# Optimization experiments

Measured on AMD Instinct MI355X. Metric: run time of the kernel, lower is better.

The kernel has to match this reference:

```python
import jax, jax.numpy as jnp
import numpy as np

N = 100000   # nodes
E = 1600000  # edges
IN = 64      # in_channels
H = 128      # hidden_features
G = 1024     # graphs in batch
NUM_REST = 3 # num_layers (extra GraphConv layers)


def setup_inputs() -> dict:
    key = jax.random.key(0)
    ks = jax.random.split(key, 12)
    x = jax.random.normal(ks[0], (N, IN), jnp.float32)
    edge_index = jax.random.randint(ks[1], (2, E), 0, N)
    edge_attr = jax.random.uniform(ks[2], (E,), jnp.float32)
    batch = jnp.sort(jax.random.randint(ks[3], (N,), 0, G))

    def glorot(k, shape, fan_in):
        return jax.random.normal(k, shape, jnp.float32) / np.float32(np.sqrt(fan_in))

    # GraphConv layer 0: in -> hidden (lin_root: no bias, lin_rel: bias)
    W_root0 = glorot(ks[4], (H, IN), IN)
    W_rel0 = glorot(ks[5], (H, IN), IN)
    b0 = jnp.zeros((H,), jnp.float32)
    # GraphConv layers 1..3: hidden -> hidden (stacked)
    W_root_r = glorot(ks[6], (NUM_REST, H, H), H)
    W_rel_r = glorot(ks[7], (NUM_REST, H, H), H)
    b_r = jnp.zeros((NUM_REST, H), jnp.float32)
    # MLPReadout: [H -> H//2 -> 1]
    Wr1 = glorot(ks[8], (H // 2, H), H)
    br1 = jnp.zeros((H // 2,), jnp.float32)
    Wr2 = glorot(ks[9], (1, H // 2), H // 2)
    br2 = jnp.zeros((1,), jnp.float32)
    return dict(x=x, edge_index=edge_index, edge_attr=edge_attr, batch=batch,
                W_root0=W_root0, W_rel0=W_rel0, b0=b0,
                W_root_r=W_root_r, W_rel_r=W_rel_r, b_r=b_r,
                Wr1=Wr1, br1=br1, Wr2=Wr2, br2=br2)


def graph_conv(x, src, dst, ew, W_root, W_rel, b):
    # PyG GraphConv (aggr='add'):
    #   out_i = W_rel @ sum_{j->i} e_ji * x_j + b + W_root @ x_i
    msg = ew[:, None] * x[src]                                   # [E, d]
    agg = jax.ops.segment_sum(msg, dst, num_segments=x.shape[0])  # [N, d]
    return agg @ W_rel.T + b + x @ W_root.T


def reference(x, edge_index, edge_attr, batch,
              W_root0, W_rel0, b0, W_root_r, W_rel_r, b_r,
              Wr1, br1, Wr2, br2):
    src, dst = edge_index[0], edge_index[1]
    y = graph_conv(x, src, dst, edge_attr, W_root0, W_rel0, b0)
    for l in range(W_root_r.shape[0]):
        y = graph_conv(y, src, dst, edge_attr, W_root_r[l], W_rel_r[l], b_r[l])
    # MLPReadout: Linear -> ReLU -> Linear
    y = jax.nn.relu(y @ Wr1.T + br1)
    y = y @ Wr2.T + br2                                           # [N, 1]
    # scatter-mean over graph assignment
    num = jax.ops.segment_sum(y, batch, num_segments=G)           # [G, 1]
    cnt = jax.ops.segment_sum(jnp.ones((y.shape[0], 1), y.dtype), batch,
                              num_segments=G)
    return num / jnp.maximum(cnt, 1.0)                            # [G, 1]
```

## Files before the change

### kernel.cpp

```cpp
#include <hip/hip_runtime.h>
#include <hip/hip_fp16.h>
#include <cstdint>
#include <cstddef>

#define NNODES 100000
#define NEDGES 1600000
#define NGRAPH 1024
#define NB_SCAN ((NNODES + 255) / 256)
#define FILL_CHUNK 4096
#define FILL_NCHUNK ((NEDGES + FILL_CHUNK - 1) / FILL_CHUNK)
#define SHARD 12500

typedef __attribute__((ext_vector_type(8))) short short8;
typedef __attribute__((ext_vector_type(8))) unsigned short ushort8;
typedef __attribute__((ext_vector_type(4))) float f32x4;

__device__ inline float b2f(unsigned short u) {
  return __uint_as_float(((unsigned int)u) << 16);
}
__device__ inline unsigned short f2b(float f) {
  unsigned int x = __float_as_uint(f);
  x += 0x7fffu + ((x >> 16) & 1u);
  return (unsigned short)(x >> 16);
}
__device__ inline unsigned int pack_edge(int src, float w) {
  unsigned short hb = __half_as_ushort(__float2half_rn(w));
  return ((unsigned int)src << 15) | ((unsigned int)hb >> 1);
}
__device__ inline void unpack_edge(unsigned int p, int& src, float& w) {
  src = (int)(p >> 15);
  w = __half2float(__ushort_as_half((unsigned short)((p & 0x7fffu) << 1)));
}

__global__ __launch_bounds__(256) void prepack_kernel(
    const float* __restrict__ Wrel0, const float* __restrict__ Wroot0,
    const float* __restrict__ WrelR, const float* __restrict__ WrootR,
    const float* __restrict__ Wr1, unsigned short* __restrict__ dst)
{
  int g = blockIdx.x * 256 + threadIdx.x;
  if (g >= 15360) return;
  const float* src; int H, K, r; unsigned short* out;
  if (g < 1024)       { src = Wrel0;  H = 128; K = 64;  r = g;        out = dst + r * 8; }
  else if (g < 2048)  { src = Wroot0; H = 128; K = 64;  r = g - 1024; out = dst + 8192 + r * 8; }
  else if (g < 8192)  { int m = g - 2048; int l = m / 2048; r = m % 2048;
                        src = WrelR + l * 16384;  H = 128; K = 128;
                        out = dst + 16384 + l * 16384 + r * 8; }
  else if (g < 14336) { int m = g - 8192; int l = m / 2048; r = m % 2048;
                        src = WrootR + l * 16384; H = 128; K = 128;
                        out = dst + 65536 + l * 16384 + r * 8; }
  else                { src = Wr1;    H = 64;  K = 128; r = g - 14336; out = dst + 114688 + r * 8; }
  int n = r % H, k8 = r / H;
  const float* s = src + (size_t)n * K + k8 * 8;
#pragma unroll
  for (int j = 0; j < 8; j++) out[j] = f2b(s[j]);
}

__global__ __launch_bounds__(256) void cvt_x_kernel(
    const float* __restrict__ x, unsigned short* __restrict__ xb)
{
  int i = blockIdx.x * 256 + threadIdx.x;
  if (i * 4 >= NNODES * 64) return;
  float4 v = *(const float4*)(x + i * 4);
  ushort4 o;
  o.x = f2b(v.x); o.y = f2b(v.y); o.z = f2b(v.z); o.w = f2b(v.w);
  *(ushort4*)(xb + i * 4) = o;
}

__global__ __launch_bounds__(256) void hist_kernel(
    const int* __restrict__ ei, int* __restrict__ deg)
{
  int e = blockIdx.x * 256 + threadIdx.x;
  if (e < NEDGES) atomicAdd(&deg[ei[NEDGES + e]], 1);
}

__global__ __launch_bounds__(256) void scan1_kernel(
    const int* __restrict__ deg, int* __restrict__ exloc, int* __restrict__ bsum)
{
  __shared__ int s[256];
  int i = blockIdx.x * 256 + threadIdx.x;
  int v = (i < NNODES) ? deg[i] : 0;
  s[threadIdx.x] = v;
  __syncthreads();
#pragma unroll
  for (int off = 1; off < 256; off <<= 1) {
    int t = (threadIdx.x >= off) ? s[threadIdx.x - off] : 0;
    __syncthreads();
    s[threadIdx.x] += t;
    __syncthreads();
  }
  if (i < NNODES) exloc[i] = s[threadIdx.x] - v;
  if (threadIdx.x == 255) bsum[blockIdx.x] = s[255];
}

__global__ __launch_bounds__(512) void scan2_kernel(int* __restrict__ bsum)
{
  __shared__ int s[512];
  int v = (threadIdx.x < NB_SCAN) ? bsum[threadIdx.x] : 0;
  s[threadIdx.x] = v;
  __syncthreads();
#pragma unroll
  for (int off = 1; off < 512; off <<= 1) {
    int t = (threadIdx.x >= off) ? s[threadIdx.x - off] : 0;
    __syncthreads();
    s[threadIdx.x] += t;
    __syncthreads();
  }
  if (threadIdx.x < NB_SCAN) bsum[threadIdx.x] = s[threadIdx.x] - v;
}

__global__ __launch_bounds__(256) void scan3_kernel(
    const int* __restrict__ exloc, const int* __restrict__ bsum,
    int* __restrict__ row_ptr, int* __restrict__ row_fill)
{
  int i = blockIdx.x * 256 + threadIdx.x;
  if (i < NNODES) {
    int v = exloc[i] + bsum[blockIdx.x];
    row_ptr[i] = v;
    row_fill[i] = v;
  }
  if (i == 0) row_ptr[NNODES] = NEDGES;
}

__global__ __launch_bounds__(256) void fill_kernel(
    const int* __restrict__ ei, const float* __restrict__ ew,
    int* __restrict__ row_fill, unsigned int* __restrict__ epack)
{
  int chunk = blockIdx.x >> 3;
  int shard = blockIdx.x & 7;
  int base = chunk * FILL_CHUNK;
  for (int t = threadIdx.x; t < FILL_CHUNK; t += 256) {
    int e = base + t;
    if (e >= NEDGES) break;
    int d = ei[NEDGES + e];
    if ((unsigned)d / SHARD == (unsigned)shard) {
      int p = atomicAdd(&row_fill[d], 1);
      epack[p] = pack_edge(ei[e], ew[e]);
    }
  }
}

__global__ __launch_bounds__(256) void gptr_kernel(
    const int* __restrict__ batch, int* __restrict__ gptr)
{
  int i = blockIdx.x * 256 + threadIdx.x;
  if (i >= NNODES) return;
  int b = batch[i];
  int bn = (i + 1 < NNODES) ? batch[i + 1] : NGRAPH;
  for (int g = b + 1; g <= bn; g++) gptr[g] = i + 1;
  if (i == 0) for (int g = 0; g <= b; g++) gptr[g] = 0;
}

__global__ __launch_bounds__(256) void agg128_kernel(
    const int* __restrict__ row_ptr, const unsigned int* __restrict__ epack,
    const unsigned short* __restrict__ x, unsigned short* __restrict__ agg)
{
  int node = blockIdx.x * 4 + (threadIdx.x >> 6);
  int lane = threadIdx.x & 63;
  if (node >= NNODES) return;
  int q = lane >> 4, sl = lane & 15;
  int s = row_ptr[node], e = row_ptr[node + 1];
  float acc[8];
#pragma unroll
  for (int j = 0; j < 8; j++) acc[j] = 0.f;

  for (int i = s + q; i < e; i += 16) {
    unsigned int p0 = epack[i];
    unsigned int p1 = (i + 4  < e) ? epack[i + 4]  : 0u;
    unsigned int p2 = (i + 8  < e) ? epack[i + 8]  : 0u;
    unsigned int p3 = (i + 12 < e) ? epack[i + 12] : 0u;
    int s0, s1, s2, s3; float w0, w1, w2, w3;
    unpack_edge(p0, s0, w0);
    unpack_edge(p1, s1, w1);
    unpack_edge(p2, s2, w2);
    unpack_edge(p3, s3, w3);
    ushort8 r0 = *(const ushort8*)(x + (size_t)s0 * 128 + sl * 8);
    ushort8 r1 = *(const ushort8*)(x + (size_t)s1 * 128 + sl * 8);
    ushort8 r2 = *(const ushort8*)(x + (size_t)s2 * 128 + sl * 8);
    ushort8 r3 = *(const ushort8*)(x + (size_t)s3 * 128 + sl * 8);
#pragma unroll
    for (int j = 0; j < 8; j++)
      acc[j] += w0 * b2f(r0[j]) + w1 * b2f(r1[j]) +
                w2 * b2f(r2[j]) + w3 * b2f(r3[j]);
  }
#pragma unroll
  for (int j = 0; j < 8; j++) {
    acc[j] += __shfl_xor(acc[j], 16, 64);
    acc[j] += __shfl_xor(acc[j], 32, 64);
  }
  if (q == 0) {
    ushort8 o;
#pragma unroll
    for (int j = 0; j < 8; j++) o[j] = f2b(acc[j]);
    *(ushort8*)(agg + (size_t)node * 128 + sl * 8) = o;
  }
}

__global__ __launch_bounds__(256) void agg64_kernel(
    const int* __restrict__ row_ptr, const unsigned int* __restrict__ epack,
    const unsigned short* __restrict__ x, unsigned short* __restrict__ agg)
{
  int node = blockIdx.x * 4 + (threadIdx.x >> 6);
  int lane = threadIdx.x & 63;
  if (node >= NNODES) return;
  int q = lane >> 3, sl = lane & 7;
  int s = row_ptr[node], e = row_ptr[node + 1];
  float acc[8];
#pragma unroll
  for (int j = 0; j < 8; j++) acc[j] = 0.f;

  for (int i = s + q; i < e; i += 16) {
    unsigned int p0 = epack[i];
    unsigned int p1 = (i + 8 < e) ? epack[i + 8] : 0u;
    int s0, s1; float w0, w1;
    unpack_edge(p0, s0, w0);
    unpack_edge(p1, s1, w1);
    ushort8 r0 = *(const ushort8*)(x + (size_t)s0 * 64 + sl * 8);
    ushort8 r1 = *(const ushort8*)(x + (size_t)s1 * 64 + sl * 8);
#pragma unroll
    for (int j = 0; j < 8; j++)
      acc[j] += w0 * b2f(r0[j]) + w1 * b2f(r1[j]);
  }
#pragma unroll
  for (int j = 0; j < 8; j++) {
    acc[j] += __shfl_xor(acc[j], 8, 64);
    acc[j] += __shfl_xor(acc[j], 16, 64);
    acc[j] += __shfl_xor(acc[j], 32, 64);
  }
  if (q == 0) {
    ushort8 o;
#pragma unroll
    for (int j = 0; j < 8; j++) o[j] = f2b(acc[j]);
    *(ushort8*)(agg + (size_t)node * 64 + sl * 8) = o;
  }
}

template <int KDIM, int HOUT, int MT, bool DUAL, bool RELU>
__global__ __launch_bounds__(256) void mfma_gemm(
    const unsigned short* __restrict__ A1, const unsigned short* __restrict__ W1,
    const unsigned short* __restrict__ A2, const unsigned short* __restrict__ W2,
    const float* __restrict__ bias, unsigned short* __restrict__ out)
{
  constexpr int NT2 = HOUT / 16;
  constexpr int KC = KDIM / 32;
  const int wave = threadIdx.x >> 6, lane = threadIdx.x & 63;
  const int quad = lane >> 4, l16 = lane & 15;
  const int n0 = (blockIdx.x * 4 + wave) * (MT * 16);

  f32x4 acc[MT][NT2];
#pragma unroll
  for (int m = 0; m < MT; m++)
#pragma unroll
    for (int t = 0; t < NT2; t++) acc[m][t] = (f32x4){0.f, 0.f, 0.f, 0.f};

  int nodes[MT];
#pragma unroll
  for (int m = 0; m < MT; m++) {
    int nd = n0 + m * 16 + l16;
    nodes[m] = nd < NNODES ? nd : NNODES - 1;
  }

#pragma unroll
  for (int c = 0; c < KC; c++) {
    short8 bfr[NT2];
#pragma unroll
    for (int t = 0; t < NT2; t++)
      bfr[t] = *(const short8*)(W1 + ((size_t)(c * 4 + quad) * HOUT + t * 16 + l16) * 8);
#pragma unroll
    for (int m = 0; m < MT; m++) {
      short8 af = *(const short8*)(A1 + (size_t)nodes[m] * KDIM + c * 32 + quad * 8);
#pragma unroll
      for (int t = 0; t < NT2; t++)
        acc[m][t] = __builtin_amdgcn_mfma_f32_16x16x32_bf16(af, bfr[t], acc[m][t], 0, 0, 0);
    }
    if (DUAL) {
#pragma unroll
      for (int t = 0; t < NT2; t++)
        bfr[t] = *(const short8*)(W2 + ((size_t)(c * 4 + quad) * HOUT + t * 16 + l16) * 8);
#pragma unroll
      for (int m = 0; m < MT; m++) {
        short8 af = *(const short8*)(A2 + (size_t)nodes[m] * KDIM + c * 32 + quad * 8);
#pragma unroll
        for (int t = 0; t < NT2; t++)
          acc[m][t] = __builtin_amdgcn_mfma_f32_16x16x32_bf16(af, bfr[t], acc[m][t], 0, 0, 0);
      }
    }
  }

#pragma unroll
  for (int m = 0; m < MT; m++) {
    int rowbase = n0 + m * 16 + quad * 4;
#pragma unroll
    for (int t = 0; t < NT2; t++) {
      float b = bias[t * 16 + l16];
#pragma unroll
      for (int r = 0; r < 4; r++) {
        int nd = rowbase + r;
        if (nd < NNODES) {
          float v = acc[m][t][r] + b;
          if (RELU) v = fmaxf(v, 0.f);
          out[(size_t)nd * HOUT + t * 16 + l16] = f2b(v);
        }
      }
    }
  }
}

__global__ __launch_bounds__(256) void readout_reduce_kernel(
    const unsigned short* __restrict__ h, const float* __restrict__ Wr2,
    const float* __restrict__ br2, const int* __restrict__ gptr,
    float* __restrict__ out)
{
  __shared__ float wsum[4];
  int g = blockIdx.x;
  int s = gptr[g], e = gptr[g + 1];
  int wave = threadIdx.x >> 6, lane = threadIdx.x & 63;
  float w2 = Wr2[lane];
  float acc = 0.f;
  for (int n = s + wave; n < e; n += 4)
    acc += b2f(h[(size_t)n * 64 + lane]) * w2;
#pragma unroll
  for (int off = 32; off >= 1; off >>= 1) acc += __shfl_xor(acc, off, 64);
  if (lane == 0) wsum[wave] = acc;
  __syncthreads();
  if (threadIdx.x == 0) {
    float cnt = (float)(e - s);
    float sum = wsum[0] + wsum[1] + wsum[2] + wsum[3] + cnt * br2[0];
    out[g] = sum / fmaxf(cnt, 1.f);
  }
}

extern "C" void kernel_launch(void* const* d_in, const int* in_sizes, int n_in,
                              void* d_out, int out_size, void* d_ws, size_t ws_size,
                              hipStream_t stream)
{
  const float* x      = (const float*)d_in[0];
  const int*   ei     = (const int*)d_in[1];
  const float* ew     = (const float*)d_in[2];
  const int*   batch  = (const int*)d_in[3];
  const float* Wroot0 = (const float*)d_in[4];
  const float* Wrel0  = (const float*)d_in[5];
  const float* b0     = (const float*)d_in[6];
  const float* WrootR = (const float*)d_in[7];
  const float* WrelR  = (const float*)d_in[8];
  const float* bR     = (const float*)d_in[9];
  const float* Wr1    = (const float*)d_in[10];
  const float* br1    = (const float*)d_in[11];
  const float* Wr2    = (const float*)d_in[12];
  const float* br2    = (const float*)d_in[13];

  char* ws = (char*)d_ws;
  unsigned short* wp   = (unsigned short*)ws;
  unsigned short* xb   = wp + 131072;
  unsigned short* agg0 = xb + (size_t)NNODES * 64;
  unsigned short* bufA = agg0 + (size_t)NNODES * 64;
  unsigned short* bufB = bufA + (size_t)NNODES * 128;
  unsigned short* hbuf = bufB + (size_t)NNODES * 128;
  int*  deg      = (int*)(hbuf + (size_t)NNODES * 64);
  int*  exloc    = deg + NNODES;
  int*  row_ptr  = exloc + NNODES;
  int*  row_fill = row_ptr + NNODES + 2;
  int*  bsum     = row_fill + NNODES;
  int*  gptr     = bsum + 512;
  unsigned int* epack = (unsigned int*)(gptr + NGRAPH + 2);

  prepack_kernel<<<60, 256, 0, stream>>>(Wrel0, Wroot0, WrelR, WrootR, Wr1, wp);
  cvt_x_kernel<<<(NNODES * 64 / 4 + 255) / 256, 256, 0, stream>>>(x, xb);

  const unsigned short* pWrel0  = wp;
  const unsigned short* pWroot0 = wp + 8192;
  const unsigned short* pWrelR  = wp + 16384;
  const unsigned short* pWrootR = wp + 65536;
  const unsigned short* pWr1    = wp + 114688;

  hipMemsetAsync(deg, 0, NNODES * sizeof(int), stream);
  hist_kernel<<<(NEDGES + 255) / 256, 256, 0, stream>>>(ei, deg);
  scan1_kernel<<<NB_SCAN, 256, 0, stream>>>(deg, exloc, bsum);
  scan2_kernel<<<1, 512, 0, stream>>>(bsum);
  scan3_kernel<<<NB_SCAN, 256, 0, stream>>>(exloc, bsum, row_ptr, row_fill);
  fill_kernel<<<FILL_NCHUNK * 8, 256, 0, stream>>>(ei, ew, row_fill, epack);
  gptr_kernel<<<(NNODES + 255) / 256, 256, 0, stream>>>(batch, gptr);

  agg64_kernel<<<(NNODES + 3) / 4, 256, 0, stream>>>(row_ptr, epack, xb, agg0);
  mfma_gemm<64, 128, 2, true, false><<<(NNODES + 127) / 128, 256, 0, stream>>>(
      agg0, pWrel0, xb, pWroot0, b0, bufB);

  unsigned short* bufs[2] = { bufB, bufA };
  for (int l = 0; l < 3; l++) {
    unsigned short* in  = bufs[l & 1];
    unsigned short* agg = bufs[(l & 1) ^ 1];
    agg128_kernel<<<(NNODES + 3) / 4, 256, 0, stream>>>(row_ptr, epack, in, agg);
    mfma_gemm<128, 128, 2, true, false><<<(NNODES + 127) / 128, 256, 0, stream>>>(
        agg, pWrelR + l * 16384, in, pWrootR + l * 16384, bR + l * 128, agg);
  }

  mfma_gemm<128, 64, 4, false, true><<<(NNODES + 255) / 256, 256, 0, stream>>>(
      bufA, pWr1, nullptr, nullptr, br1, hbuf);
  readout_reduce_kernel<<<NGRAPH, 256, 0, stream>>>(hbuf, Wr2, br2, gptr, (float*)d_out);
}
```

Measured before the change: 596.4 us.

## Replace atomic CSR build with two-level bucket counting sort

Swaps the global-atomic histogram, three-pass scan and sharded atomic fill for a two-level counting sort. Edges are first binned into 256-node buckets using per-chunk shared-memory histograms, then scattered to bucket order as (dst, packed) records, and finally each bucket is sorted locally in shared memory to produce row_ptr and epack. This targets global atomic contention and the 8x redundant edge reads of the old sharded fill. In exchange it adds a single-block scan over about 153K counters and a temporary record buffer that reuses bufA.

Measured after the change: 757.2 us. 1.27x slower.

```diff
diff --git a/kernel.cpp b/kernel.cpp
--- a/kernel.cpp
+++ b/kernel.cpp
@@ -6,10 +6,14 @@
 #define NNODES 100000
 #define NEDGES 1600000
 #define NGRAPH 1024
-#define NB_SCAN ((NNODES + 255) / 256)
-#define FILL_CHUNK 4096
-#define FILL_NCHUNK ((NEDGES + FILL_CHUNK - 1) / FILL_CHUNK)
-#define SHARD 12500
+
+#define BK 256
+#define NBUCKET 391
+#define CHUNK 4096
+#define NCHUNK 391
+#define NBE (NBUCKET * NCHUNK)
+#define SCAN_T 1024
+#define PER_T ((NBE + SCAN_T - 1) / SCAN_T)
 
 typedef __attribute__((ext_vector_type(8))) short short8;
 typedef __attribute__((ext_vector_type(8))) unsigned short ushort8;
@@ -66,76 +70,96 @@
   *(ushort4*)(xb + i * 4) = o;
 }
 
-__global__ __launch_bounds__(256) void hist_kernel(
-    const int* __restrict__ ei, int* __restrict__ deg)
-{
-  int e = blockIdx.x * 256 + threadIdx.x;
-  if (e < NEDGES) atomicAdd(&deg[ei[NEDGES + e]], 1);
-}
-
-__global__ __launch_bounds__(256) void scan1_kernel(
-    const int* __restrict__ deg, int* __restrict__ exloc, int* __restrict__ bsum)
-{
+__global__ __launch_bounds__(256) void bucket_count_kernel(
+    const int* __restrict__ ei, int* __restrict__ cnt)
+{
+  __shared__ int hist[NBUCKET];
+  for (int i = threadIdx.x; i < NBUCKET; i += 256) hist[i] = 0;
+  __syncthreads();
+  int base = blockIdx.x * CHUNK;
+  for (int t = threadIdx.x; t < CHUNK; t += 256) {
+    int e = base + t;
+    if (e < NEDGES) atomicAdd(&hist[ei[NEDGES + e] >> 8], 1);
+  }
+  __syncthreads();
+  for (int i = threadIdx.x; i < NBUCKET; i += 256)
+    cnt[i * NCHUNK + blockIdx.x] = hist[i];
+}
+
+__global__ __launch_bounds__(SCAN_T) void bucket_scan_kernel(int* __restrict__ cnt)
+{
+  __shared__ int s[SCAN_T];
+  int t = threadIdx.x;
+  int lo = t * PER_T, hi = lo + PER_T; if (hi > NBE) hi = NBE;
+  int sum = 0;
+  for (int i = lo; i < hi; i++) sum += cnt[i];
+  s[t] = sum;
+  __syncthreads();
+#pragma unroll
+  for (int off = 1; off < SCAN_T; off <<= 1) {
+    int v = (t >= off) ? s[t - off] : 0;
+    __syncthreads();
+    s[t] += v;
+    __syncthreads();
+  }
+  int run = s[t] - sum;
+  for (int i = lo; i < hi; i++) { int v = cnt[i]; cnt[i] = run; run += v; }
+}
+
+__global__ __launch_bounds__(256) void bucket_scatter_kernel(
+    const int* __restrict__ ei, const float* __restrict__ ew,
+    const int* __restrict__ basepos, uint2* __restrict__ rec)
+{
+  __shared__ int pos[NBUCKET];
+  for (int i = threadIdx.x; i < NBUCKET; i += 256)
+    pos[i] = basepos[i * NCHUNK + blockIdx.x];
+  __syncthreads();
+  int base = blockIdx.x * CHUNK;
+  for (int t = threadIdx.x; t < CHUNK; t += 256) {
+    int e = base + t;
+    if (e < NEDGES) {
+      int d = ei[NEDGES + e];
+      int p = atomicAdd(&pos[d >> 8], 1);
+      rec[p] = make_uint2((unsigned int)d, pack_edge(ei[e], ew[e]));
+    }
+  }
+}
+
+__global__ __launch_bounds__(256) void bucket_fill_kernel(
+    const int* __restrict__ basepos, const uint2* __restrict__ rec,
+    unsigned int* __restrict__ epack, int* __restrict__ row_ptr)
+{
+  __shared__ int off[BK];
   __shared__ int s[256];
-  int i = blockIdx.x * 256 + threadIdx.x;
-  int v = (i < NNODES) ? deg[i] : 0;
-  s[threadIdx.x] = v;
-  __syncthreads();
-#pragma unroll
-  for (int off = 1; off < 256; off <<= 1) {
-    int t = (threadIdx.x >= off) ? s[threadIdx.x - off] : 0;
+  int b = blockIdx.x, t = threadIdx.x;
+  int start = basepos[b * NCHUNK];
+  int end = (b + 1 < NBUCKET) ? basepos[(b + 1) * NCHUNK] : NEDGES;
+  int nbase = b * BK;
+  off[t] = 0;
+  __syncthreads();
+  for (int i = start + t; i < end; i += 256)
+    atomicAdd(&off[rec[i].x - nbase], 1);
+  __syncthreads();
+  int v = off[t];
+  s[t] = v;
+  __syncthreads();
+#pragma unroll
+  for (int o = 1; o < 256; o <<= 1) {
+    int u = (t >= o) ? s[t - o] : 0;
     __syncthreads();
-    s[threadIdx.x] += t;
+    s[t] += u;
     __syncthreads();
   }
-  if (i < NNODES) exloc[i] = s[threadIdx.x] - v;
-  if (threadIdx.x == 255) bsum[blockIdx.x] = s[255];
-}
-
-__global__ __launch_bounds__(512) void scan2_kernel(int* __restrict__ bsum)
-{
-  __shared__ int s[512];
-  int v = (threadIdx.x < NB_SCAN) ? bsum[threadIdx.x] : 0;
-  s[threadIdx.x] = v;
-  __syncthreads();
-#pragma unroll
-  for (int off = 1; off < 512; off <<= 1) {
-    int t = (threadIdx.x >= off) ? s[threadIdx.x - off] : 0;
-    __syncthreads();
-    s[threadIdx.x] += t;
-    __syncthreads();
-  }
-  if (threadIdx.x < NB_SCAN) bsum[threadIdx.x] = s[threadIdx.x] - v;
-}
-
-__global__ __launch_bounds__(256) void scan3_kernel(
-    const int* __restrict__ exloc, const int* __restrict__ bsum,
-    int* __restrict__ row_ptr, int* __restrict__ row_fill)
-{
-  int i = blockIdx.x * 256 + threadIdx.x;
-  if (i < NNODES) {
-    int v = exloc[i] + bsum[blockIdx.x];
-    row_ptr[i] = v;
-    row_fill[i] = v;
-  }
-  if (i == 0) row_ptr[NNODES] = NEDGES;
-}
-
-__global__ __launch_bounds__(256) void fill_kernel(
-    const int* __restrict__ ei, const float* __restrict__ ew,
-    int* __restrict__ row_fill, unsigned int* __restrict__ epack)
-{
-  int chunk = blockIdx.x >> 3;
-  int shard = blockIdx.x & 7;
-  int base = chunk * FILL_CHUNK;
-  for (int t = threadIdx.x; t < FILL_CHUNK; t += 256) {
-    int e = base + t;
-    if (e >= NEDGES) break;
-    int d = ei[NEDGES + e];
-    if ((unsigned)d / SHARD == (unsigned)shard) {
-      int p = atomicAdd(&row_fill[d], 1);
-      epack[p] = pack_edge(ei[e], ew[e]);
-    }
+  int ex = s[t] - v;
+  int g = nbase + t;
+  if (g <= NNODES) row_ptr[g] = start + ex;
+  __syncthreads();
+  off[t] = ex;
+  __syncthreads();
+  for (int i = start + t; i < end; i += 256) {
+    uint2 r = rec[i];
+    int lp = atomicAdd(&off[r.x - nbase], 1);
+    epack[start + lp] = r.y;
   }
 }
 
@@ -355,13 +379,11 @@
   unsigned short* bufA = agg0 + (size_t)NNODES * 64;
   unsigned short* bufB = bufA + (size_t)NNODES * 128;
   unsigned short* hbuf = bufB + (size_t)NNODES * 128;
-  int*  deg      = (int*)(hbuf + (size_t)NNODES * 64);
-  int*  exloc    = deg + NNODES;
-  int*  row_ptr  = exloc + NNODES;
-  int*  row_fill = row_ptr + NNODES + 2;
-  int*  bsum     = row_fill + NNODES;
-  int*  gptr     = bsum + 512;
+  int*  cnt      = (int*)(hbuf + (size_t)NNODES * 64);
+  int*  row_ptr  = cnt + ((NBE + 63) & ~63);
+  int*  gptr     = row_ptr + NNODES + 2;
   unsigned int* epack = (unsigned int*)(gptr + NGRAPH + 2);
+  uint2* rec = (uint2*)bufA;
 
   prepack_kernel<<<60, 256, 0, stream>>>(Wrel0, Wroot0, WrelR, WrootR, Wr1, wp);
   cvt_x_kernel<<<(NNODES * 64 / 4 + 255) / 256, 256, 0, stream>>>(x, xb);
@@ -372,12 +394,10 @@
   const unsigned short* pWrootR = wp + 65536;
   const unsigned short* pWr1    = wp + 114688;
 
-  hipMemsetAsync(deg, 0, NNODES * sizeof(int), stream);
-  hist_kernel<<<(NEDGES + 255) / 256, 256, 0, stream>>>(ei, deg);
-  scan1_kernel<<<NB_SCAN, 256, 0, stream>>>(deg, exloc, bsum);
-  scan2_kernel<<<1, 512, 0, stream>>>(bsum);
-  scan3_kernel<<<NB_SCAN, 256, 0, stream>>>(exloc, bsum, row_ptr, row_fill);
-  fill_kernel<<<FILL_NCHUNK * 8, 256, 0, stream>>>(ei, ew, row_fill, epack);
+  bucket_count_kernel<<<NCHUNK, 256, 0, stream>>>(ei, cnt);
+  bucket_scan_kernel<<<1, SCAN_T, 0, stream>>>(cnt);
+  bucket_scatter_kernel<<<NCHUNK, 256, 0, stream>>>(ei, ew, cnt, rec);
+  bucket_fill_kernel<<<NBUCKET, 256, 0, stream>>>(cnt, rec, epack, row_ptr);
   gptr_kernel<<<(NNODES + 255) / 256, 256, 0, stream>>>(batch, gptr);
 
   agg64_kernel<<<(NNODES + 3) / 4, 256, 0, stream>>>(row_ptr, epack, xb, agg0);
```
